# Kernel tuning notes

Measured on AMD Instinct MI355X. Metric: run time of the kernel, lower is better.

Reference implementation:

```python
import jax, jax.numpy as jnp
import numpy as np

ALPHA = 0.2  # LeakyReLU negative slope
MASK_VAL = -1e9


def setup_inputs() -> dict:
    key = jax.random.key(0)
    k1, k2, k3, k4 = jax.random.split(key, 4)
    B, N, F_in, F_out = 8, 2048, 512, 512
    h = jax.random.normal(k1, (B, N, F_in), dtype=jnp.float32)
    adj = jax.random.randint(k2, (B, N, N), 0, 2, dtype=jnp.int32)
    # xavier_uniform with gain=1.414
    def xavier(k, shape, gain=1.414):
        fan_in, fan_out = shape[0], shape[1]
        bound = gain * np.sqrt(6.0 / (fan_in + fan_out))
        return jax.random.uniform(k, shape, jnp.float32, -bound, bound)
    W = xavier(k3, (F_in, F_out))
    a = xavier(k4, (2 * F_out, 1))
    return {"h": h, "adj": adj, "W": W, "a": a}


def reference(h, adj, W, a):
    # h: [B,N,Fin], adj: [B,N,N], W: [Fin,Fout], a: [2*Fout,1]
    Fout = W.shape[1]
    Wh = jnp.matmul(h, W)  # [B,N,Fout]
    # Split 'a' into source/target halves: concat([Wh_i, Wh_j]) @ a
    #   == (Wh_i @ a1) + (Wh_j @ a2), avoiding the O(N^2*2F) concat tensor.
    a1 = a[:Fout, 0]   # [Fout]
    a2 = a[Fout:, 0]   # [Fout]
    e_i = jnp.einsum('bnf,f->bn', Wh, a1)  # [B,N] score contribution of node i
    e_j = jnp.einsum('bnf,f->bn', Wh, a2)  # [B,N] score contribution of node j
    e = e_i[:, :, None] + e_j[:, None, :]  # [B,N,N]
    e = jax.nn.leaky_relu(e, negative_slope=ALPHA)
    e = jnp.where(adj == 0, MASK_VAL, e)
    attention = jax.nn.softmax(e, axis=2)  # [B,N,N]
    h_prime = jnp.matmul(attention, Wh)    # [B,N,Fout]
    return jax.nn.elu(h_prime)
```

## Files before the change

### kernel.cpp

```cpp
#include <hip/hip_runtime.h>
#include <hip/hip_bf16.h>

#define ALPHA 0.2f
#define LOG2E 1.44269504088896340736f

typedef float  f32x4 __attribute__((ext_vector_type(4)));
typedef float  f32x2 __attribute__((ext_vector_type(2)));
typedef int    i32x4 __attribute__((ext_vector_type(4)));
typedef int    i32x2 __attribute__((ext_vector_type(2)));
typedef unsigned int u32x2 __attribute__((ext_vector_type(2)));

static __device__ __forceinline__ void mfma_bf16_16x16x32(f32x4& c, i32x4 a, i32x4 b) {
  asm("v_mfma_f32_16x16x32_bf16 %0, %1, %2, %0" : "+v"(c) : "v"(a), "v"(b));
}
static __device__ __forceinline__ unsigned short f2bf(float x) {
  __hip_bfloat16 b = __float2bfloat16(x);
  return *reinterpret_cast<unsigned short*>(&b);
}
static __device__ __forceinline__ unsigned int cvtpk(float lo, float hi) {
  unsigned int r;
  asm("v_cvt_pk_bf16_f32 %0, %1, %2" : "=v"(r) : "v"(lo), "v"(hi));
  return r;
}
static __device__ __forceinline__ float dot4(f32x4 a, f32x4 b) {
  return a.x*b.x + a.y*b.y + a.z*b.z + a.w*b.w;
}

__global__ __launch_bounds__(256) void k_setup(const float* __restrict__ W, const float* __restrict__ a,
                                               unsigned short* __restrict__ wt,
                                               float* __restrict__ v1, float* __restrict__ v2,
                                               float* __restrict__ eiej) {
  const int bid = blockIdx.x, tid = threadIdx.x;
  __shared__ float S[32][33];
  if (bid < 256) {
    const int k0 = (bid >> 4) * 32, f0 = (bid & 15) * 32;
    const int r = tid >> 5, c = tid & 31;
    #pragma unroll
    for (int rr = r; rr < 32; rr += 8) S[rr][c] = W[(size_t)(k0 + rr) * 512 + f0 + c];
    __syncthreads();
    #pragma unroll
    for (int rr = r; rr < 32; rr += 8) wt[(size_t)(f0 + rr) * 512 + k0 + c] = f2bf(S[c][rr]);
  } else if (bid < 384) {
    const int kk = (bid - 256) * 4 + (tid >> 6);
    const int l = tid & 63;
    const float* wr = W + (size_t)kk * 512 + l * 8;
    f32x4 w0 = *(const f32x4*)(wr),            w1 = *(const f32x4*)(wr + 4);
    f32x4 p0 = *(const f32x4*)(a + l*8),       p1 = *(const f32x4*)(a + l*8 + 4);
    f32x4 q0 = *(const f32x4*)(a + 512 + l*8), q1 = *(const f32x4*)(a + 512 + l*8 + 4);
    float s1 = dot4(w0,p0) + dot4(w1,p1);
    float s2 = dot4(w0,q0) + dot4(w1,q1);
    #pragma unroll
    for (int off = 1; off < 64; off <<= 1) { s1 += __shfl_xor(s1, off); s2 += __shfl_xor(s2, off); }
    if (l == 0) { v1[kk] = s1 * LOG2E; v2[kk] = s2 * LOG2E; }
  } else {
    const int idx = (bid - 384) * 1024 + tid * 4;
    *(f32x4*)(eiej + idx) = (f32x4){0.f,0.f,0.f,0.f};
  }
}

__global__ __launch_bounds__(256) void k_prep(const float* __restrict__ h,
                                              const float* __restrict__ v1, const float* __restrict__ v2,
                                              unsigned short* __restrict__ hT,
                                              float* __restrict__ ei, float* __restrict__ ej) {
  const int bid = blockIdx.x, tid = threadIdx.x;
  const int ft = bid & 15, nt = (bid >> 4) & 63, b = bid >> 10;
  __shared__ __align__(16) float S[32][36];

  const int n_loc = tid >> 3, fq = (tid & 7) * 4;
  const f32x4 v = __builtin_nontemporal_load(
      (const f32x4*)(h + (size_t)(b*2048 + nt*32 + n_loc)*512 + ft*32 + fq));
  *(f32x4*)&S[n_loc][fq] = v;

  const f32x4 a1 = *(const f32x4*)(v1 + ft*32 + fq);
  const f32x4 a2 = *(const f32x4*)(v2 + ft*32 + fq);
  float s1 = dot4(v, a1), s2 = dot4(v, a2);
  #pragma unroll
  for (int off = 1; off < 8; off <<= 1) { s1 += __shfl_xor(s1, off); s2 += __shfl_xor(s2, off); }
  if ((tid & 7) == 0) {
    atomicAdd(&ei[b*2048 + nt*32 + n_loc], s1);
    atomicAdd(&ej[b*2048 + nt*32 + n_loc], s2);
  }
  __syncthreads();

  const int f_loc = tid >> 3, nq = (tid & 7) * 4;
  u32x2 pk;
  pk.x = cvtpk(S[nq+0][f_loc], S[nq+1][f_loc]);
  pk.y = cvtpk(S[nq+2][f_loc], S[nq+3][f_loc]);
  *(u32x2*)(hT + (size_t)(b*512 + ft*32 + f_loc)*2048 + nt*32 + nq) = pk;
}

__global__ __launch_bounds__(512, 2) void k_attn(const int* __restrict__ adj,
                                                 const unsigned short* __restrict__ hT,
                                                 const float* __restrict__ ei, const float* __restrict__ ej,
                                                 unsigned short* __restrict__ C1) {
  const int tid = threadIdx.x;
  const int w = tid >> 6, l = tid & 63;
  const int fl = l & 15, kq = l >> 4;
  const int b = blockIdx.x & 7;
  const int i0 = (blockIdx.x >> 3) * 64;

  __shared__ __align__(16) float ejl[2048];
  __shared__ __align__(16) unsigned char abits[2][64][64];
  __shared__ __align__(16) float llds[64];

  for (int idx = tid; idx < 2048; idx += 512) ejl[idx] = ej[b*2048 + idx];

  float eir[4];
  #pragma unroll
  for (int fr = 0; fr < 4; ++fr) eir[fr] = ei[b*2048 + i0 + fr*16 + fl];

  const unsigned short* bp[4];
  #pragma unroll
  for (int cf = 0; cf < 4; ++cf)
    bp[cf] = hT + (size_t)(b*512 + w*64 + cf*16 + fl) * 2048 + kq*8;

  const int srow0 = tid >> 4, srow1 = 32 + (tid >> 4), stw = tid & 15;
  const int* agp0 = adj + (size_t)(b*2048 + i0 + srow0) * 2048 + stw*32;
  const int* agp1 = adj + (size_t)(b*2048 + i0 + srow1) * 2048 + stw*32;
  const int wa0 = srow0*64 + ((stw*4 + 4*srow0) & 63);
  const int wa1 = srow1*64 + ((stw*4 + 4*srow1) & 63);

  f32x4 acc[4][4];
  #pragma unroll
  for (int i = 0; i < 4; ++i)
    #pragma unroll
    for (int j = 0; j < 4; ++j) acc[i][j] = (f32x4){0.f,0.f,0.f,0.f};
  float s[4] = {0.f, 0.f, 0.f, 0.f};

  i32x4 bcur[4], bnxt[4];
  #pragma unroll
  for (int cf = 0; cf < 4; ++cf) bcur[cf] = *(const i32x4*)(bp[cf]);

  i32x4 va[16];
  #pragma unroll
  for (int q = 0; q < 8; ++q) {
    va[q]   = __builtin_nontemporal_load((const i32x4*)(agp0 + q*4));
    va[8+q] = __builtin_nontemporal_load((const i32x4*)(agp1 + q*4));
  }
  {
    unsigned int b0 = 0, b1 = 0;
    #pragma unroll
    for (int q = 0; q < 8; ++q)
      #pragma unroll
      for (int e = 0; e < 4; ++e) {
        b0 |= ((unsigned)va[q][e]   & 1u) << (q*4 + e);
        b1 |= ((unsigned)va[8+q][e] & 1u) << (q*4 + e);
      }
    *(unsigned int*)(&abits[0][0][0] + wa0) = b0;
    *(unsigned int*)(&abits[0][0][0] + wa1) = b1;
  }
  __syncthreads();

  for (int c = 0; c < 4; ++c) {
    const int cur = c & 1;
    if (c < 3) {
      const int jo = (c + 1) * 512;
      #pragma unroll
      for (int q = 0; q < 8; ++q) {
        va[q]   = __builtin_nontemporal_load((const i32x4*)(agp0 + jo + q*4));
        va[8+q] = __builtin_nontemporal_load((const i32x4*)(agp1 + jo + q*4));
      }
    }
    for (int tl = 0; tl < 16; ++tl) {
      const int t = c*16 + tl;
      if (t < 63) {
        #pragma unroll
        for (int cf = 0; cf < 4; ++cf) bnxt[cf] = *(const i32x4*)(bp[cf] + (t+1)*32);
      }
      const f32x4 ej0 = *(const f32x4*)&ejl[t*32 + kq*8];
      const f32x4 ej1 = *(const f32x4*)&ejl[t*32 + kq*8 + 4];
      const int ao = (tl*4 + kq + 4*fl) & 63;
      i32x4 af[4];
      #pragma unroll
      for (int fr = 0; fr < 4; ++fr) {
        const unsigned int byt = abits[cur][fr*16 + fl][ao];
        float p[8];
        #pragma unroll
        for (int e = 0; e < 8; ++e) {
          float ee = eir[fr] + ((e < 4) ? ej0[e] : ej1[e-4]);
          ee = fmaxf(ee, ALPHA * ee);
          const float pv = __builtin_amdgcn_exp2f(ee);
          p[e] = (byt & (1u << e)) ? pv : 0.f;
          s[fr] += p[e];
        }
        af[fr] = (i32x4){ (int)cvtpk(p[0],p[1]), (int)cvtpk(p[2],p[3]),
                          (int)cvtpk(p[4],p[5]), (int)cvtpk(p[6],p[7]) };
      }
      #pragma unroll
      for (int fr = 0; fr < 4; ++fr)
        #pragma unroll
        for (int cf = 0; cf < 4; ++cf)
          mfma_bf16_16x16x32(acc[fr][cf], af[fr], bcur[cf]);
      #pragma unroll
      for (int cf = 0; cf < 4; ++cf) bcur[cf] = bnxt[cf];
    }
    if (c < 3) {
      unsigned int b0 = 0, b1 = 0;
      #pragma unroll
      for (int q = 0; q < 8; ++q)
        #pragma unroll
        for (int e = 0; e < 4; ++e) {
          b0 |= ((unsigned)va[q][e]   & 1u) << (q*4 + e);
          b1 |= ((unsigned)va[8+q][e] & 1u) << (q*4 + e);
        }
      *(unsigned int*)(&abits[cur ^ 1][0][0] + wa0) = b0;
      *(unsigned int*)(&abits[cur ^ 1][0][0] + wa1) = b1;
    }
    __syncthreads();
  }

  #pragma unroll
  for (int fr = 0; fr < 4; ++fr) {
    s[fr] += __shfl_xor(s[fr], 16);
    s[fr] += __shfl_xor(s[fr], 32);
  }
  if (w == 0 && kq == 0) {
    #pragma unroll
    for (int fr = 0; fr < 4; ++fr) llds[fr*16 + fl] = s[fr];
  }
  __syncthreads();
  asm volatile("s_nop 7\ns_nop 7\ns_nop 7" :::);

  #pragma unroll
  for (int fr = 0; fr < 4; ++fr) {
    const f32x4 lv = *(const f32x4*)&llds[fr*16 + kq*4];
    f32x4 inv;
    inv.x = __builtin_amdgcn_rcpf(lv.x); inv.y = __builtin_amdgcn_rcpf(lv.y);
    inv.z = __builtin_amdgcn_rcpf(lv.z); inv.w = __builtin_amdgcn_rcpf(lv.w);
    #pragma unroll
    for (int cf = 0; cf < 4; ++cf) {
      const int f = w*64 + cf*16 + fl;
      unsigned short* cp = C1 + (size_t)(b*2048 + i0 + fr*16 + kq*4) * 512 + f;
      cp[0]    = f2bf(acc[fr][cf].x * inv.x);
      cp[512]  = f2bf(acc[fr][cf].y * inv.y);
      cp[1024] = f2bf(acc[fr][cf].z * inv.z);
      cp[1536] = f2bf(acc[fr][cf].w * inv.w);
    }
  }
}

__global__ __launch_bounds__(512, 2) void k_gemm2(const unsigned short* __restrict__ C1,
                                                  const unsigned short* __restrict__ wt,
                                                  float* __restrict__ out) {
  const int tid = threadIdx.x;
  const int w = tid >> 6, l = tid & 63;
  const int fl = l & 15, kq = l >> 4;
  const int row0 = (blockIdx.x & 7) * 2048 + (blockIdx.x >> 3) * 64;

  const unsigned short* ap[4];
  const unsigned short* bp[4];
  #pragma unroll
  for (int fr = 0; fr < 4; ++fr) ap[fr] = C1 + (size_t)(row0 + fr*16 + fl)*512 + kq*8;
  #pragma unroll
  for (int cf = 0; cf < 4; ++cf) bp[cf] = wt + (size_t)(w*64 + cf*16 + fl)*512 + kq*8;

  f32x4 acc[4][4];
  #pragma unroll
  for (int i = 0; i < 4; ++i)
    #pragma unroll
    for (int j = 0; j < 4; ++j) acc[i][j] = (f32x4){0.f,0.f,0.f,0.f};

  i32x4 ac[4], bc[4], an[4], bn[4];
  #pragma unroll
  for (int x = 0; x < 4; ++x) { ac[x] = *(const i32x4*)(ap[x]); bc[x] = *(const i32x4*)(bp[x]); }

  for (int sI = 0; sI < 16; ++sI) {
    const int sn = (sI < 15) ? sI + 1 : 15;
    #pragma unroll
    for (int x = 0; x < 4; ++x) {
      an[x] = *(const i32x4*)(ap[x] + sn*32);
      bn[x] = *(const i32x4*)(bp[x] + sn*32);
    }
    #pragma unroll
    for (int fr = 0; fr < 4; ++fr)
      #pragma unroll
      for (int cf = 0; cf < 4; ++cf)
        mfma_bf16_16x16x32(acc[fr][cf], ac[fr], bc[cf]);
    #pragma unroll
    for (int x = 0; x < 4; ++x) { ac[x] = an[x]; bc[x] = bn[x]; }
  }

  asm volatile("s_nop 7\ns_nop 7\ns_nop 7" :::);
  #pragma unroll
  for (int fr = 0; fr < 4; ++fr)
    #pragma unroll
    for (int cf = 0; cf < 4; ++cf) {
      const int f = w*64 + cf*16 + fl;
      float* op = out + (size_t)(row0 + fr*16 + kq*4) * 512 + f;
      const f32x4 v = acc[fr][cf];
      float o0 = v.x > 0.f ? v.x : __builtin_amdgcn_exp2f(v.x * LOG2E) - 1.f;
      float o1 = v.y > 0.f ? v.y : __builtin_amdgcn_exp2f(v.y * LOG2E) - 1.f;
      float o2 = v.z > 0.f ? v.z : __builtin_amdgcn_exp2f(v.z * LOG2E) - 1.f;
      float o3 = v.w > 0.f ? v.w : __builtin_amdgcn_exp2f(v.w * LOG2E) - 1.f;
      __builtin_nontemporal_store(o0, op);
      __builtin_nontemporal_store(o1, op + 512);
      __builtin_nontemporal_store(o2, op + 1024);
      __builtin_nontemporal_store(o3, op + 1536);
    }
}

extern "C" void kernel_launch(void* const* d_in, const int* in_sizes, int n_in,
                              void* d_out, int out_size, void* d_ws, size_t ws_size,
                              hipStream_t stream) {
  const float* h  = (const float*)d_in[0];
  const int*  adj = (const int*)d_in[1];
  const float* W  = (const float*)d_in[2];
  const float* a  = (const float*)d_in[3];
  float* out = (float*)d_out;
  char* ws = (char*)d_ws;
  unsigned short* wt = (unsigned short*)(ws);
  unsigned short* hT = (unsigned short*)(ws + 524288);
  unsigned short* C1 = (unsigned short*)(ws + 17301504);
  float* ei = (float*)(ws + 34078720);
  float* ej = (float*)(ws + 34144256);
  float* v1 = (float*)(ws + 34209792);
  float* v2 = (float*)(ws + 34211840);

  hipLaunchKernelGGL(k_setup, dim3(416),  dim3(256), 0, stream, W, a, wt, v1, v2, ei);
  hipLaunchKernelGGL(k_prep,  dim3(8192), dim3(256), 0, stream, h, v1, v2, hT, ei, ej);
  hipLaunchKernelGGL(k_attn,  dim3(256),  dim3(512), 0, stream, adj, hT, ei, ej, C1);
  hipLaunchKernelGGL(k_gemm2, dim3(256),  dim3(512), 0, stream, C1, wt, out);
}
```

Baseline: 390.4 us.

## Restructure attention kernel: 32-row tiles, shared-memory P staging, double-buffered phases

Halves the attention row tile from 64 to 32 rows and doubles the grid to 512 blocks, with launch bounds raised to 4 blocks per SM. Each P element is now computed exactly once by one thread and written as bf16 into a swizzled, double-buffered LDS tile. MFMA waves then read A fragments from that tile, so the bit-packing of adj and the redundant exp work across waves go away. The aim is more occupancy and less duplicated exp/VALU work. In exchange, each block reloads the full hT B-operand for only 32 rows, which doubles hT traffic, and the extra barriers add synchronisation cost.

Result: faster. 362.7 us (-7.1%).

```diff
diff --git a/kernel.cpp b/kernel.cpp
--- a/kernel.cpp
+++ b/kernel.cpp
@@ -89,7 +89,7 @@
   *(u32x2*)(hT + (size_t)(b*512 + ft*32 + f_loc)*2048 + nt*32 + nq) = pk;
 }
 
-__global__ __launch_bounds__(512, 2) void k_attn(const int* __restrict__ adj,
+__global__ __launch_bounds__(512, 4) void k_attn(const int* __restrict__ adj,
                                                  const unsigned short* __restrict__ hT,
                                                  const float* __restrict__ ei, const float* __restrict__ ej,
                                                  unsigned short* __restrict__ C1) {
@@ -97,132 +97,121 @@
   const int w = tid >> 6, l = tid & 63;
   const int fl = l & 15, kq = l >> 4;
   const int b = blockIdx.x & 7;
-  const int i0 = (blockIdx.x >> 3) * 64;
-
+  const int i0 = (blockIdx.x >> 3) * 32;
+
+  __shared__ __align__(16) unsigned short Plds[2][4096];
   __shared__ __align__(16) float ejl[2048];
-  __shared__ __align__(16) unsigned char abits[2][64][64];
-  __shared__ __align__(16) float llds[64];
-
-  for (int idx = tid; idx < 2048; idx += 512) ejl[idx] = ej[b*2048 + idx];
-
-  float eir[4];
-  #pragma unroll
-  for (int fr = 0; fr < 4; ++fr) eir[fr] = ei[b*2048 + i0 + fr*16 + fl];
+  __shared__ __align__(16) float llds[32];
+
+  *(f32x4*)&ejl[tid*4] = *(const f32x4*)(ej + b*2048 + tid*4);
+
+  const int prow = w*4 + (l >> 4);
+  const int pj   = (l & 15) * 8;
+  const float eir = ei[b*2048 + i0 + prow];
+  const int* aptr = adj + ((size_t)(b*2048 + i0 + prow) << 11) + pj;
+  const int wboff = prow*256 + ((pj*2) ^ ((prow & 7) << 4));
 
   const unsigned short* bp[4];
   #pragma unroll
   for (int cf = 0; cf < 4; ++cf)
     bp[cf] = hT + (size_t)(b*512 + w*64 + cf*16 + fl) * 2048 + kq*8;
-
-  const int srow0 = tid >> 4, srow1 = 32 + (tid >> 4), stw = tid & 15;
-  const int* agp0 = adj + (size_t)(b*2048 + i0 + srow0) * 2048 + stw*32;
-  const int* agp1 = adj + (size_t)(b*2048 + i0 + srow1) * 2048 + stw*32;
-  const int wa0 = srow0*64 + ((stw*4 + 4*srow0) & 63);
-  const int wa1 = srow1*64 + ((stw*4 + 4*srow1) & 63);
-
-  f32x4 acc[4][4];
-  #pragma unroll
-  for (int i = 0; i < 4; ++i)
+  const int zz = ((kq ^ (fl & 7)) << 4);
+  const int arow0 = fl * 256, arow1 = (16 + fl) * 256;
+
+  f32x4 acc[2][4];
+  #pragma unroll
+  for (int i = 0; i < 2; ++i)
     #pragma unroll
     for (int j = 0; j < 4; ++j) acc[i][j] = (f32x4){0.f,0.f,0.f,0.f};
-  float s[4] = {0.f, 0.f, 0.f, 0.f};
-
-  i32x4 bcur[4], bnxt[4];
+  float sum = 0.f;
+
+  i32x4 bcur[4];
   #pragma unroll
   for (int cf = 0; cf < 4; ++cf) bcur[cf] = *(const i32x4*)(bp[cf]);
 
-  i32x4 va[16];
-  #pragma unroll
-  for (int q = 0; q < 8; ++q) {
-    va[q]   = __builtin_nontemporal_load((const i32x4*)(agp0 + q*4));
-    va[8+q] = __builtin_nontemporal_load((const i32x4*)(agp1 + q*4));
-  }
-  {
-    unsigned int b0 = 0, b1 = 0;
-    #pragma unroll
-    for (int q = 0; q < 8; ++q)
-      #pragma unroll
-      for (int e = 0; e < 4; ++e) {
-        b0 |= ((unsigned)va[q][e]   & 1u) << (q*4 + e);
-        b1 |= ((unsigned)va[8+q][e] & 1u) << (q*4 + e);
+  i32x4 pfa0 = __builtin_nontemporal_load((const i32x4*)(aptr));
+  i32x4 pfa1 = __builtin_nontemporal_load((const i32x4*)(aptr + 4));
+  i32x4 pfb0 = __builtin_nontemporal_load((const i32x4*)(aptr + 128));
+  i32x4 pfb1 = __builtin_nontemporal_load((const i32x4*)(aptr + 128 + 4));
+
+#define P_PHASE(BUFI, S, A0, A1) do {                                          \
+    const f32x4 e0 = *(const f32x4*)&ejl[(S)*128 + pj];                        \
+    const f32x4 e1 = *(const f32x4*)&ejl[(S)*128 + pj + 4];                    \
+    float p[8];                                                                \
+    _Pragma("unroll")                                                          \
+    for (int e = 0; e < 8; ++e) {                                              \
+      float x = eir + ((e < 4) ? e0[e] : e1[e-4]);                             \
+      x = fmaxf(x, ALPHA * x);                                                 \
+      const float pv = __builtin_amdgcn_exp2f(x);                              \
+      const int av = (e < 4) ? (A0)[e] : (A1)[e-4];                            \
+      p[e] = av ? pv : 0.f;                                                    \
+      sum += p[e];                                                             \
+    }                                                                          \
+    i32x4 pk;                                                                  \
+    pk.x = (int)cvtpk(p[0],p[1]); pk.y = (int)cvtpk(p[2],p[3]);                \
+    pk.z = (int)cvtpk(p[4],p[5]); pk.w = (int)cvtpk(p[6],p[7]);                \
+    *(i32x4*)((char*)&Plds[BUFI][0] + wboff) = pk;                             \
+  } while (0)
+
+#define MFMA_STEP(BUFI, S) do {                                                \
+    const char* pb = (const char*)&Plds[BUFI][0];                              \
+    _Pragma("unroll")                                                          \
+    for (int kk = 0; kk < 4; ++kk) {                                           \
+      const int t = (S)*4 + kk;                                                \
+      const int tn = (t < 63) ? t + 1 : 63;                                    \
+      i32x4 bnxt[4];                                                           \
+      _Pragma("unroll")                                                        \
+      for (int cf = 0; cf < 4; ++cf) bnxt[cf] = *(const i32x4*)(bp[cf] + tn*32); \
+      const i32x4 af0 = *(const i32x4*)(pb + arow0 + ((kk << 6) ^ zz));        \
+      const i32x4 af1 = *(const i32x4*)(pb + arow1 + ((kk << 6) ^ zz));        \
+      _Pragma("unroll")                                                        \
+      for (int cf = 0; cf < 4; ++cf) {                                         \
+        mfma_bf16_16x16x32(acc[0][cf], af0, bcur[cf]);                         \
+        mfma_bf16_16x16x32(acc[1][cf], af1, bcur[cf]);                         \
+      }                                                                        \
+      _Pragma("unroll")                                                        \
+      for (int cf = 0; cf < 4; ++cf) bcur[cf] = bnxt[cf];                      \
+    }                                                                          \
+  } while (0)
+
+  __syncthreads();
+  P_PHASE(0, 0, pfa0, pfa1);
+  pfa0 = __builtin_nontemporal_load((const i32x4*)(aptr + 2*128));
+  pfa1 = __builtin_nontemporal_load((const i32x4*)(aptr + 2*128 + 4));
+  __syncthreads();
+
+  for (int ss = 0; ss < 8; ++ss) {
+    const int s0 = ss*2, s1 = ss*2 + 1;
+    MFMA_STEP(0, s0);
+    P_PHASE(1, s0 + 1, pfb0, pfb1);
+    if (s0 + 3 < 16) {
+      pfb0 = __builtin_nontemporal_load((const i32x4*)(aptr + (s0+3)*128));
+      pfb1 = __builtin_nontemporal_load((const i32x4*)(aptr + (s0+3)*128 + 4));
+    }
+    __syncthreads();
+    MFMA_STEP(1, s1);
+    if (s1 < 15) {
+      P_PHASE(0, s1 + 1, pfa0, pfa1);
+      if (s1 + 3 < 16) {
+        pfa0 = __builtin_nontemporal_load((const i32x4*)(aptr + (s1+3)*128));
+        pfa1 = __builtin_nontemporal_load((const i32x4*)(aptr + (s1+3)*128 + 4));
       }
-    *(unsigned int*)(&abits[0][0][0] + wa0) = b0;
-    *(unsigned int*)(&abits[0][0][0] + wa1) = b1;
-  }
-  __syncthreads();
-
-  for (int c = 0; c < 4; ++c) {
-    const int cur = c & 1;
-    if (c < 3) {
-      const int jo = (c + 1) * 512;
-      #pragma unroll
-      for (int q = 0; q < 8; ++q) {
-        va[q]   = __builtin_nontemporal_load((const i32x4*)(agp0 + jo + q*4));
-        va[8+q] = __builtin_nontemporal_load((const i32x4*)(agp1 + jo + q*4));
-      }
-    }
-    for (int tl = 0; tl < 16; ++tl) {
-      const int t = c*16 + tl;
-      if (t < 63) {
-        #pragma unroll
-        for (int cf = 0; cf < 4; ++cf) bnxt[cf] = *(const i32x4*)(bp[cf] + (t+1)*32);
-      }
-      const f32x4 ej0 = *(const f32x4*)&ejl[t*32 + kq*8];
-      const f32x4 ej1 = *(const f32x4*)&ejl[t*32 + kq*8 + 4];
-      const int ao = (tl*4 + kq + 4*fl) & 63;
-      i32x4 af[4];
-      #pragma unroll
-      for (int fr = 0; fr < 4; ++fr) {
-        const unsigned int byt = abits[cur][fr*16 + fl][ao];
-        float p[8];
-        #pragma unroll
-        for (int e = 0; e < 8; ++e) {
-          float ee = eir[fr] + ((e < 4) ? ej0[e] : ej1[e-4]);
-          ee = fmaxf(ee, ALPHA * ee);
-          const float pv = __builtin_amdgcn_exp2f(ee);
-          p[e] = (byt & (1u << e)) ? pv : 0.f;
-          s[fr] += p[e];
-        }
-        af[fr] = (i32x4){ (int)cvtpk(p[0],p[1]), (int)cvtpk(p[2],p[3]),
-                          (int)cvtpk(p[4],p[5]), (int)cvtpk(p[6],p[7]) };
-      }
-      #pragma unroll
-      for (int fr = 0; fr < 4; ++fr)
-        #pragma unroll
-        for (int cf = 0; cf < 4; ++cf)
-          mfma_bf16_16x16x32(acc[fr][cf], af[fr], bcur[cf]);
-      #pragma unroll
-      for (int cf = 0; cf < 4; ++cf) bcur[cf] = bnxt[cf];
-    }
-    if (c < 3) {
-      unsigned int b0 = 0, b1 = 0;
-      #pragma unroll
-      for (int q = 0; q < 8; ++q)
-        #pragma unroll
-        for (int e = 0; e < 4; ++e) {
-          b0 |= ((unsigned)va[q][e]   & 1u) << (q*4 + e);
-          b1 |= ((unsigned)va[8+q][e] & 1u) << (q*4 + e);
-        }
-      *(unsigned int*)(&abits[cur ^ 1][0][0] + wa0) = b0;
-      *(unsigned int*)(&abits[cur ^ 1][0][0] + wa1) = b1;
     }
     __syncthreads();
   }
-
-  #pragma unroll
-  for (int fr = 0; fr < 4; ++fr) {
-    s[fr] += __shfl_xor(s[fr], 16);
-    s[fr] += __shfl_xor(s[fr], 32);
-  }
-  if (w == 0 && kq == 0) {
-    #pragma unroll
-    for (int fr = 0; fr < 4; ++fr) llds[fr*16 + fl] = s[fr];
-  }
+#undef P_PHASE
+#undef MFMA_STEP
+
+  sum += __shfl_xor(sum, 1);
+  sum += __shfl_xor(sum, 2);
+  sum += __shfl_xor(sum, 4);
+  sum += __shfl_xor(sum, 8);
+  if ((l & 15) == 0) llds[prow] = sum;
   __syncthreads();
   asm volatile("s_nop 7\ns_nop 7\ns_nop 7" :::);
 
   #pragma unroll
-  for (int fr = 0; fr < 4; ++fr) {
+  for (int fr = 0; fr < 2; ++fr) {
     const f32x4 lv = *(const f32x4*)&llds[fr*16 + kq*4];
     f32x4 inv;
     inv.x = __builtin_amdgcn_rcpf(lv.x); inv.y = __builtin_amdgcn_rcpf(lv.y);
@@ -318,6 +307,6 @@
 
   hipLaunchKernelGGL(k_setup, dim3(416),  dim3(256), 0, stream, W, a, wt, v1, v2, ei);
   hipLaunchKernelGGL(k_prep,  dim3(8192), dim3(256), 0, stream, h, v1, v2, hT, ei, ej);
-  hipLaunchKernelGGL(k_attn,  dim3(256),  dim3(512), 0, stream, adj, hT, ei, ej, C1);
+  hipLaunchKernelGGL(k_attn,  dim3(512),  dim3(512), 0, stream, adj, hT, ei, ej, C1);
   hipLaunchKernelGGL(k_gemm2, dim3(256),  dim3(512), 0, stream, C1, wt, out);
 }
```
